# Kernel tuning notes

Measured on AMD Instinct MI355X. Metric: run time of the kernel, lower is better.

## Reference

```python
import jax, jax.numpy as jnp
import numpy as np

TOP_K = 4


def setup_inputs() -> dict:
    key = jax.random.key(0)
    k1, k2, k3 = jax.random.split(key, 3)
    T, H, E = 16384, 2880, 128
    hidden_states = jax.random.normal(k1, (T, H), dtype=jnp.float32)
    weight = jax.random.normal(k2, (E, H), dtype=jnp.float32) * 0.02
    bias = jax.random.normal(k3, (E,), dtype=jnp.float32) * 0.02
    return {"hidden_states": hidden_states, "weight": weight, "bias": bias}


def reference(hidden_states, weight, bias):
    # [T, H] @ [H, E] + [E] -> router logits [T, E]
    hidden_states = hidden_states.reshape(-1, weight.shape[1])
    router_logits = jnp.einsum('th,eh->te', hidden_states, weight) + bias
    # top-k over experts, then softmax over the k selected logits
    router_top_value, router_indices = jax.lax.top_k(router_logits, TOP_K)
    router_scores = jax.nn.softmax(router_top_value, axis=-1)
    return router_scores, router_indices
```

## Files before the change

kernel.cpp:

```cpp
#include <hip/hip_runtime.h>
#include <hip/hip_bf16.h>
#include <math.h>

#define T_TOKENS 16384
#define H_DIM    2880
#define KHALF    1440
#define E_EXP    128
#define TOPK     4
#define MT       32
#define MTM      64
#define KC       32
#define NCHUNK   (H_DIM / KC)
#define NCHUNK_H (KHALF / KC)
#define EPS_GAP  5e-4f

#define WS_WOFF   64
#define WS_WBYTES (NCHUNK * 1024 * 16)
#define WS_FLOFF  (WS_WOFF + WS_WBYTES)
#define WS_CAOFF  (WS_FLOFF + T_TOKENS * 4)
#define WS_NEED   (WS_CAOFF + T_TOKENS * 8)

typedef __bf16 bf16x8 __attribute__((ext_vector_type(8)));
typedef float  f32x4  __attribute__((ext_vector_type(4)));

__device__ __forceinline__ void split2(float a, float b,
                                       unsigned int& hi, unsigned int& lo) {
    float2 p; p.x = a; p.y = b;
    __hip_bfloat162 h = __float22bfloat162_rn(p);
    unsigned int hu; __builtin_memcpy(&hu, &h, 4);
    float2 r;
    r.x = a - __uint_as_float((hu & 0xffffu) << 16);
    r.y = b - __uint_as_float(hu & 0xffff0000u);
    __hip_bfloat162 l = __float22bfloat162_rn(r);
    unsigned int lu; __builtin_memcpy(&lu, &l, 4);
    hi = hu; lo = lu;
}

__global__ __launch_bounds__(256) void prep_w(const float* __restrict__ W,
                                              uint4* __restrict__ wsW) {
    const int f   = blockIdx.x * 256 + threadIdx.x;
    const int kc  = f >> 9;
    const int rem = f & 511;
    const int nt  = rem >> 6;
    const int L   = rem & 63;
    const int e   = nt * 16 + (L & 15);
    const int k   = kc * KC + (L >> 4) * 8;
    const float* p = W + (size_t)e * H_DIM + k;
    const float4 x0 = *(const float4*)p;
    const float4 x1 = *(const float4*)(p + 4);
    uint4 hi, lo;
    split2(x0.x, x0.y, hi.x, lo.x);
    split2(x0.z, x0.w, hi.y, lo.y);
    split2(x1.x, x1.y, hi.z, lo.z);
    split2(x1.z, x1.w, hi.w, lo.w);
    wsW[(size_t)kc * 1024 + nt * 64 + L]       = hi;
    wsW[(size_t)kc * 1024 + 512 + nt * 64 + L] = lo;
}

__global__ __launch_bounds__(1024, 4) void router_main(
    const float* __restrict__ A, const uint4* __restrict__ wsW,
    const float* __restrict__ bias, float* __restrict__ out,
    int* __restrict__ flag_count, int* __restrict__ flag_list,
    uint2* __restrict__ cand_list)
{
    union SMem {
        struct {
            uint4 W  [2][2][1024];
            uint4 Ahi[2][2][4][64];
            uint4 Alo[2][2][4][64];
        } s;
        float L[MTM][129];
    };
    __shared__ SMem sm;

    const int tid    = threadIdx.x;
    const int t_base = blockIdx.x * MTM;

    const int wave  = tid >> 6;
    const int L     = tid & 63;
    const int whalf = wave >> 3;
    const int wmg   = (wave >> 2) & 1;
    const int wng   = wave & 3;

    const int shalf = whalf;
    const int wv    = wave & 7;
    const uint4* wsrc = wsW + (size_t)(shalf * NCHUNK_H) * 1024 + (wv * 2) * 64 + L;

    const bool doA = tid < 512;
    const int ah   = wave & 1;
    const int awm  = (wave >> 1) & 3;
    const int akq  = L >> 4;
    const int t16  = L & 15;
    const int at   = awm * 16 + t16;
    const float* Ag = A + (size_t)(t_base + at) * H_DIM + ah * KHALF + akq * 8;

    f32x4 acc[2][2];
#pragma unroll
    for (int m = 0; m < 2; ++m)
#pragma unroll
        for (int n = 0; n < 2; ++n) { f32x4 z = {0.f, 0.f, 0.f, 0.f}; acc[m][n] = z; }

#define STAGE(NB, IT)                                                          \
    {                                                                          \
        if (doA) {                                                             \
            uint4 hi4, lo4;                                                    \
            split2(av0.x, av0.y, hi4.x, lo4.x);                                \
            split2(av0.z, av0.w, hi4.y, lo4.y);                                \
            split2(av1.x, av1.y, hi4.z, lo4.z);                                \
            split2(av1.z, av1.w, hi4.w, lo4.w);                                \
            sm.s.Ahi[NB][ah][awm][L] = hi4;                                    \
            sm.s.Alo[NB][ah][awm][L] = lo4;                                    \
        }                                                                      \
        const uint4* wc = wsrc + (size_t)(IT) * 1024;                          \
        _Pragma("unroll")                                                      \
        for (int j = 0; j < 2; ++j) {                                          \
            __builtin_amdgcn_global_load_lds(                                  \
                (const __attribute__((address_space(1))) void*)(wc + j * 64),  \
                (__attribute__((address_space(3))) void*)&sm.s.W[NB][shalf][(wv * 2 + j) * 64], \
                16, 0, 0);                                                     \
        }                                                                      \
    }

    float4 av0, av1;
    if (doA) { av0 = *(const float4*)(Ag); av1 = *(const float4*)(Ag + 4); }
    STAGE(0, 0);
    if (doA) { av0 = *(const float4*)(Ag + KC); av1 = *(const float4*)(Ag + KC + 4); }
    __syncthreads();

    int b = 0;
    for (int it = 0; it < NCHUNK_H; ++it) {
        if (it + 1 < NCHUNK_H) {
            STAGE(b ^ 1, it + 1);
            if (doA && it + 2 < NCHUNK_H) {
                av0 = *(const float4*)(Ag + (it + 2) * KC);
                av1 = *(const float4*)(Ag + (it + 2) * KC + 4);
            }
        }
        const bf16x8 ah0 = *(const bf16x8*)&sm.s.Ahi[b][whalf][wmg * 2 + 0][L];
        const bf16x8 al0 = *(const bf16x8*)&sm.s.Alo[b][whalf][wmg * 2 + 0][L];
        const bf16x8 ah1 = *(const bf16x8*)&sm.s.Ahi[b][whalf][wmg * 2 + 1][L];
        const bf16x8 al1 = *(const bf16x8*)&sm.s.Alo[b][whalf][wmg * 2 + 1][L];
#pragma unroll
        for (int n = 0; n < 2; ++n) {
            const int nt = wng * 2 + n;
            const bf16x8 whi = *(const bf16x8*)&sm.s.W[b][whalf][nt * 64 + L];
            const bf16x8 wlo = *(const bf16x8*)&sm.s.W[b][whalf][512 + nt * 64 + L];
            acc[0][n] = __builtin_amdgcn_mfma_f32_16x16x32_bf16(ah0, whi, acc[0][n], 0, 0, 0);
            acc[0][n] = __builtin_amdgcn_mfma_f32_16x16x32_bf16(ah0, wlo, acc[0][n], 0, 0, 0);
            acc[0][n] = __builtin_amdgcn_mfma_f32_16x16x32_bf16(al0, whi, acc[0][n], 0, 0, 0);
            acc[1][n] = __builtin_amdgcn_mfma_f32_16x16x32_bf16(ah1, whi, acc[1][n], 0, 0, 0);
            acc[1][n] = __builtin_amdgcn_mfma_f32_16x16x32_bf16(ah1, wlo, acc[1][n], 0, 0, 0);
            acc[1][n] = __builtin_amdgcn_mfma_f32_16x16x32_bf16(al1, whi, acc[1][n], 0, 0, 0);
        }
        __syncthreads();
        b ^= 1;
    }
#undef STAGE

    if (whalf == 0) {
#pragma unroll
        for (int m = 0; m < 2; ++m)
#pragma unroll
            for (int n = 0; n < 2; ++n) {
                const int e = (wng * 2 + n) * 16 + (L & 15);
                const float bv = bias[e];
#pragma unroll
                for (int r = 0; r < 4; ++r)
                    sm.L[(wmg * 2 + m) * 16 + (L >> 4) * 4 + r][e] = acc[m][n][r] + bv;
            }
    }
    __syncthreads();
    if (whalf == 1) {
#pragma unroll
        for (int m = 0; m < 2; ++m)
#pragma unroll
            for (int n = 0; n < 2; ++n) {
                const int e = (wng * 2 + n) * 16 + (L & 15);
#pragma unroll
                for (int r = 0; r < 4; ++r)
                    sm.L[(wmg * 2 + m) * 16 + (L >> 4) * 4 + r][e] += acc[m][n][r];
            }
    }
    __syncthreads();

    if (tid < MTM) {
        float v0 = -1e30f, v1 = -1e30f, v2 = -1e30f, v3 = -1e30f, v4 = -1e30f;
        int   i0 = 0, i1 = 0, i2 = 0, i3 = 0, i4 = 0;
        for (int e = 0; e < E_EXP; ++e) {
            const float x = sm.L[tid][e];
            if (x > v4) {
                if (x > v0)      { v4=v3;i4=i3; v3=v2;i3=i2; v2=v1;i2=i1; v1=v0;i1=i0; v0=x;i0=e; }
                else if (x > v1) { v4=v3;i4=i3; v3=v2;i3=i2; v2=v1;i2=i1; v1=x;i1=e; }
                else if (x > v2) { v4=v3;i4=i3; v3=v2;i3=i2; v2=x;i2=e; }
                else if (x > v3) { v4=v3;i4=i3; v3=x;i3=e; }
                else             { v4=x;i4=e; }
            }
        }
        const float g0 = v0 - v1, g1 = v1 - v2, g2 = v2 - v3, g3 = v3 - v4;
        float mg = g0 < g1 ? g0 : g1;
        mg = mg < g2 ? mg : g2;
        mg = mg < g3 ? mg : g3;

        const float e0x = expf(v0 - v0);
        const float e1x = expf(v1 - v0);
        const float e2x = expf(v2 - v0);
        const float e3x = expf(v3 - v0);
        const float s   = e0x + e1x + e2x + e3x;

        const int gt = t_base + tid;
        float* out_scores = out;
        float* out_idx    = out + (size_t)T_TOKENS * TOPK;
        out_scores[gt * 4 + 0] = e0x / s;
        out_scores[gt * 4 + 1] = e1x / s;
        out_scores[gt * 4 + 2] = e2x / s;
        out_scores[gt * 4 + 3] = e3x / s;
        out_idx[gt * 4 + 0] = (float)i0;
        out_idx[gt * 4 + 1] = (float)i1;
        out_idx[gt * 4 + 2] = (float)i2;
        out_idx[gt * 4 + 3] = (float)i3;

        if (mg < EPS_GAP) {
            const int p = atomicAdd(flag_count, 1);
            if (p < T_TOKENS) {
                flag_list[p] = gt;
                unsigned ids[8];
                int nc = 0;
                const float thr = v3 - EPS_GAP;
                for (int e = 0; e < E_EXP; ++e) {
                    if (sm.L[tid][e] >= thr) {
                        if (nc < 8) ids[nc] = (unsigned)e;
                        ++nc;
                    }
                }
                uint2 cd;
                if (nc > 8) {
                    cd.x = 0xFEu; cd.y = 0xFFFFFFFFu;
                } else {
                    for (int q = nc; q < 8; ++q) ids[q] = 0xFFu;
                    cd.x = ids[0] | (ids[1] << 8) | (ids[2] << 16) | (ids[3] << 24);
                    cd.y = ids[4] | (ids[5] << 8) | (ids[6] << 16) | (ids[7] << 24);
                }
                cand_list[p] = cd;
            }
        }
    }
}

__global__ __launch_bounds__(256) void router_recheck(
    const float* __restrict__ A, const float* __restrict__ W,
    const float* __restrict__ bias, float* __restrict__ out,
    const int* __restrict__ flag_count, const int* __restrict__ flag_list,
    const uint2* __restrict__ cand_list)
{
    __shared__ float  sA[H_DIM];
    __shared__ double sLog[8];
    __shared__ int    sIds[8];
    __shared__ double sPart[256];
    __shared__ double sFull[E_EXP];

    int count = *flag_count;
    if (count > T_TOKENS) count = T_TOKENS;

    const int tid = threadIdx.x;

    for (int i = blockIdx.x; i < count; i += gridDim.x) {
        const int t = flag_list[i];
        const uint2 cd = cand_list[i];
        __syncthreads();

        for (int q = tid; q < H_DIM / 4; q += 256)
            *(float4*)&sA[q * 4] = *(const float4*)(A + (size_t)t * H_DIM + q * 4);
        __syncthreads();

        const bool full = ((cd.x & 0xFFu) == 0xFEu);
        if (!full) {
            const int sl = tid >> 5;
            const int j  = tid & 31;
            const unsigned e = (sl < 4 ? (cd.x >> (sl * 8)) : (cd.y >> ((sl - 4) * 8))) & 0xFFu;
            double sum = 0.0;
            if (e < E_EXP) {
                const float* wrow = W + (size_t)e * H_DIM;
                for (int k = j; k < H_DIM; k += 32)
                    sum += (double)sA[k] * (double)wrow[k];
            }
#pragma unroll
            for (int off = 16; off > 0; off >>= 1)
                sum += __shfl_down(sum, off, 32);
            if (j == 0) {
                sIds[sl] = (e < E_EXP) ? (int)e : -1;
                sLog[sl] = (e < E_EXP) ? (sum + (double)bias[e]) : -1e300;
            }
            __syncthreads();
            if (tid == 0) {
                double v0 = -1e300, v1 = -1e300, v2 = -1e300, v3 = -1e300;
                int    i0 = 0, i1 = 0, i2 = 0, i3 = 0;
                for (int q = 0; q < 8; ++q) {
                    if (sIds[q] < 0) continue;
                    const double x = sLog[q];
                    const int    id = sIds[q];
                    if (x > v3) {
                        if (x > v0)      { v3=v2;i3=i2; v2=v1;i2=i1; v1=v0;i1=i0; v0=x;i0=id; }
                        else if (x > v1) { v3=v2;i3=i2; v2=v1;i2=i1; v1=x;i1=id; }
                        else if (x > v2) { v3=v2;i3=i2; v2=x;i2=id; }
                        else             { v3=x;i3=id; }
                    }
                }
                const double e0x = exp(v0 - v0);
                const double e1x = exp(v1 - v0);
                const double e2x = exp(v2 - v0);
                const double e3x = exp(v3 - v0);
                const double s   = e0x + e1x + e2x + e3x;
                float* out_scores = out;
                float* out_idx    = out + (size_t)T_TOKENS * TOPK;
                out_scores[t * 4 + 0] = (float)(e0x / s);
                out_scores[t * 4 + 1] = (float)(e1x / s);
                out_scores[t * 4 + 2] = (float)(e2x / s);
                out_scores[t * 4 + 3] = (float)(e3x / s);
                out_idx[t * 4 + 0] = (float)i0;
                out_idx[t * 4 + 1] = (float)i1;
                out_idx[t * 4 + 2] = (float)i2;
                out_idx[t * 4 + 3] = (float)i3;
            }
        } else {
            const int e = tid & (E_EXP - 1);
            const int h = tid >> 7;
            const float* wrow = W + (size_t)e * H_DIM + h * KHALF;
            const float* arow = &sA[h * KHALF];
            double s0 = 0.0, s1 = 0.0;
            for (int k = 0; k < KHALF; k += 2) {
                s0 += (double)arow[k]     * (double)wrow[k];
                s1 += (double)arow[k + 1] * (double)wrow[k + 1];
            }
            sPart[tid] = s0 + s1;
            __syncthreads();
            if (h == 0) sFull[e] = sPart[e] + sPart[e + 128] + (double)bias[e];
            __syncthreads();
            if (tid == 0) {
                double v0 = -1e300, v1 = -1e300, v2 = -1e300, v3 = -1e300;
                int    i0 = 0, i1 = 0, i2 = 0, i3 = 0;
                for (int q = 0; q < E_EXP; ++q) {
                    const double x = sFull[q];
                    if (x > v3) {
                        if (x > v0)      { v3=v2;i3=i2; v2=v1;i2=i1; v1=v0;i1=i0; v0=x;i0=q; }
                        else if (x > v1) { v3=v2;i3=i2; v2=v1;i2=i1; v1=x;i1=q; }
                        else if (x > v2) { v3=v2;i3=i2; v2=x;i2=q; }
                        else             { v3=x;i3=q; }
                    }
                }
                const double e0x = exp(v0 - v0);
                const double e1x = exp(v1 - v0);
                const double e2x = exp(v2 - v0);
                const double e3x = exp(v3 - v0);
                const double s   = e0x + e1x + e2x + e3x;
                float* out_scores = out;
                float* out_idx    = out + (size_t)T_TOKENS * TOPK;
                out_scores[t * 4 + 0] = (float)(e0x / s);
                out_scores[t * 4 + 1] = (float)(e1x / s);
                out_scores[t * 4 + 2] = (float)(e2x / s);
                out_scores[t * 4 + 3] = (float)(e3x / s);
                out_idx[t * 4 + 0] = (float)i0;
                out_idx[t * 4 + 1] = (float)i1;
                out_idx[t * 4 + 2] = (float)i2;
                out_idx[t * 4 + 3] = (float)i3;
            }
        }
        __syncthreads();
    }
}

__global__ __launch_bounds__(512, 4) void router_main_fb(
    const float* __restrict__ A, const float* __restrict__ W,
    const float* __restrict__ bias, float* __restrict__ out,
    int* __restrict__ flag_count, int* __restrict__ flag_list)
{
    __shared__ __align__(16) uint2 sAhi[2][2][128];
    __shared__ __align__(16) uint2 sAlo[2][2][128];
    __shared__ __align__(16) uint4 sWhi[2][8][64];
    __shared__ __align__(16) uint4 sWlo[2][8][64];
    __shared__ float sL[MT][129];

    const int tid    = threadIdx.x;
    const int t_base = blockIdx.x * MT;
    const int wave  = tid >> 6;
    const int L     = tid & 63;
    const int whalf = wave >> 2;
    const int wm    = wave & 1;
    const int wn    = (wave >> 1) & 1;
    const int shalf = tid >> 8;
    const int tid_h = tid & 255;
    const int at = tid_h >> 3;
    const int ac = tid_h & 7;
    const int a_idx = (at >> 4) * 128 + ((((ac >> 1) << 4) | (at & 15)) << 1) + (ac & 1);
    const float* Ag = A + (size_t)(t_base + at) * H_DIM + shalf * KHALF + ac * 4;
    const int we  = tid_h >> 1;
    const int wq0 = (tid_h & 1) * 2;
    const float* Wg = W + (size_t)we * H_DIM + shalf * KHALF + wq0 * 8;
    const int w_nt = we >> 4;
    const int w_n  = we & 15;

    uint2* sAhiF = &sAhi[shalf][0][0];
    uint2* sAloF = &sAlo[shalf][0][0];

    f32x4 acc[4];
#pragma unroll
    for (int i = 0; i < 4; ++i) { f32x4 z = {0.f, 0.f, 0.f, 0.f}; acc[i] = z; }

    for (int k0 = 0; k0 < KHALF; k0 += KC) {
        const float4 av  = *(const float4*)(Ag + k0);
        const float4 wv0 = *(const float4*)(Wg + k0);
        const float4 wv1 = *(const float4*)(Wg + k0 + 4);
        const float4 wv2 = *(const float4*)(Wg + k0 + 8);
        const float4 wv3 = *(const float4*)(Wg + k0 + 12);

        uint2 ahp, alp;
        split2(av.x, av.y, ahp.x, alp.x);
        split2(av.z, av.w, ahp.y, alp.y);
        uint4 whp0, wlp0, whp1, wlp1;
        split2(wv0.x, wv0.y, whp0.x, wlp0.x);
        split2(wv0.z, wv0.w, whp0.y, wlp0.y);
        split2(wv1.x, wv1.y, whp0.z, wlp0.z);
        split2(wv1.z, wv1.w, whp0.w, wlp0.w);
        split2(wv2.x, wv2.y, whp1.x, wlp1.x);
        split2(wv2.z, wv2.w, whp1.y, wlp1.y);
        split2(wv3.x, wv3.y, whp1.z, wlp1.z);
        split2(wv3.z, wv3.w, whp1.w, wlp1.w);

        __syncthreads();
        sAhiF[a_idx] = ahp;
        sAloF[a_idx] = alp;
        sWhi[shalf][w_nt][((wq0 + 0) << 4) | w_n] = whp0;
        sWhi[shalf][w_nt][((wq0 + 1) << 4) | w_n] = whp1;
        sWlo[shalf][w_nt][((wq0 + 0) << 4) | w_n] = wlp0;
        sWlo[shalf][w_nt][((wq0 + 1) << 4) | w_n] = wlp1;
        __syncthreads();

        const bf16x8 ahi = *(const bf16x8*)&sAhi[whalf][wm][L * 2];
        const bf16x8 alo = *(const bf16x8*)&sAlo[whalf][wm][L * 2];
#pragma unroll
        for (int i = 0; i < 4; ++i) {
            const int nt = wn * 4 + i;
            const bf16x8 whi = *(const bf16x8*)&sWhi[whalf][nt][L];
            const bf16x8 wlo = *(const bf16x8*)&sWlo[whalf][nt][L];
            acc[i] = __builtin_amdgcn_mfma_f32_16x16x32_bf16(ahi, whi, acc[i], 0, 0, 0);
            acc[i] = __builtin_amdgcn_mfma_f32_16x16x32_bf16(ahi, wlo, acc[i], 0, 0, 0);
            acc[i] = __builtin_amdgcn_mfma_f32_16x16x32_bf16(alo, whi, acc[i], 0, 0, 0);
        }
    }

    __syncthreads();
    if (whalf == 0) {
#pragma unroll
        for (int i = 0; i < 4; ++i) {
            const int e = wn * 64 + i * 16 + (L & 15);
            const float b = bias[e];
#pragma unroll
            for (int r = 0; r < 4; ++r)
                sL[wm * 16 + (L >> 4) * 4 + r][e] = acc[i][r] + b;
        }
    }
    __syncthreads();
    if (whalf == 1) {
#pragma unroll
        for (int i = 0; i < 4; ++i) {
            const int e = wn * 64 + i * 16 + (L & 15);
#pragma unroll
            for (int r = 0; r < 4; ++r)
                sL[wm * 16 + (L >> 4) * 4 + r][e] += acc[i][r];
        }
    }
    __syncthreads();

    if (tid < MT) {
        float v0 = -1e30f, v1 = -1e30f, v2 = -1e30f, v3 = -1e30f, v4 = -1e30f;
        int   i0 = 0, i1 = 0, i2 = 0, i3 = 0, i4 = 0;
        for (int e = 0; e < E_EXP; ++e) {
            const float x = sL[tid][e];
            if (x > v4) {
                if (x > v0)      { v4=v3;i4=i3; v3=v2;i3=i2; v2=v1;i2=i1; v1=v0;i1=i0; v0=x;i0=e; }
                else if (x > v1) { v4=v3;i4=i3; v3=v2;i3=i2; v2=v1;i2=i1; v1=x;i1=e; }
                else if (x > v2) { v4=v3;i4=i3; v3=v2;i3=i2; v2=x;i2=e; }
                else if (x > v3) { v4=v3;i4=i3; v3=x;i3=e; }
                else             { v4=x;i4=e; }
            }
        }
        const float g0 = v0 - v1, g1 = v1 - v2, g2 = v2 - v3, g3 = v3 - v4;
        float mg = g0 < g1 ? g0 : g1;
        mg = mg < g2 ? mg : g2;
        mg = mg < g3 ? mg : g3;

        const float e0x = expf(v0 - v0);
        const float e1x = expf(v1 - v0);
        const float e2x = expf(v2 - v0);
        const float e3x = expf(v3 - v0);
        const float s   = e0x + e1x + e2x + e3x;

        const int gt = t_base + tid;
        float* out_scores = out;
        float* out_idx    = out + (size_t)T_TOKENS * TOPK;
        out_scores[gt * 4 + 0] = e0x / s;
        out_scores[gt * 4 + 1] = e1x / s;
        out_scores[gt * 4 + 2] = e2x / s;
        out_scores[gt * 4 + 3] = e3x / s;
        out_idx[gt * 4 + 0] = (float)i0;
        out_idx[gt * 4 + 1] = (float)i1;
        out_idx[gt * 4 + 2] = (float)i2;
        out_idx[gt * 4 + 3] = (float)i3;

        if (mg < EPS_GAP) {
            const int p = atomicAdd(flag_count, 1);
            if (p < T_TOKENS) flag_list[p] = gt;
        }
    }
}

__global__ __launch_bounds__(256) void router_recheck_fb(
    const float* __restrict__ A, const float* __restrict__ W,
    const float* __restrict__ bias, float* __restrict__ out,
    const int* __restrict__ flag_count, const int* __restrict__ flag_list)
{
    __shared__ double sPart[256];
    __shared__ double sLog[E_EXP];

    int count = *flag_count;
    if (count > T_TOKENS) count = T_TOKENS;

    const int tid = threadIdx.x;
    const int e   = tid & (E_EXP - 1);
    const int h   = tid >> 7;

    for (int i = blockIdx.x; i < count; i += gridDim.x) {
        const int t = flag_list[i];
        const float* arow = A + (size_t)t * H_DIM + h * KHALF;
        const float* wrow = W + (size_t)e * H_DIM + h * KHALF;

        double s0 = 0.0, s1 = 0.0, s2 = 0.0, s3 = 0.0;
        float4 a[8], w[8];
#pragma unroll
        for (int q = 0; q < 8; ++q) {
            a[q] = *(const float4*)(arow + q * 4);
            w[q] = *(const float4*)(wrow + q * 4);
        }
        for (int it = 0; it < KHALF / 32 - 1; ++it) {
            const float* ap = arow + (it + 1) * 32;
            const float* wp = wrow + (it + 1) * 32;
            float4 na[8], nw[8];
#pragma unroll
            for (int q = 0; q < 8; ++q) {
                na[q] = *(const float4*)(ap + q * 4);
                nw[q] = *(const float4*)(wp + q * 4);
            }
#pragma unroll
            for (int q = 0; q < 8; ++q) {
                s0 += (double)a[q].x * (double)w[q].x;
                s1 += (double)a[q].y * (double)w[q].y;
                s2 += (double)a[q].z * (double)w[q].z;
                s3 += (double)a[q].w * (double)w[q].w;
            }
#pragma unroll
            for (int q = 0; q < 8; ++q) { a[q] = na[q]; w[q] = nw[q]; }
        }
#pragma unroll
        for (int q = 0; q < 8; ++q) {
            s0 += (double)a[q].x * (double)w[q].x;
            s1 += (double)a[q].y * (double)w[q].y;
            s2 += (double)a[q].z * (double)w[q].z;
            s3 += (double)a[q].w * (double)w[q].w;
        }
        sPart[tid] = (s0 + s1) + (s2 + s3);
        __syncthreads();
        if (h == 0) sLog[e] = sPart[e] + sPart[e + 128] + (double)bias[e];
        __syncthreads();

        if (tid == 0) {
            double v0 = -1e300, v1 = -1e300, v2 = -1e300, v3 = -1e300;
            int    i0 = 0, i1 = 0, i2 = 0, i3 = 0;
            for (int q = 0; q < E_EXP; ++q) {
                const double x = sLog[q];
                if (x > v3) {
                    if (x > v0)      { v3=v2;i3=i2; v2=v1;i2=i1; v1=v0;i1=i0; v0=x;i0=q; }
                    else if (x > v1) { v3=v2;i3=i2; v2=v1;i2=i1; v1=x;i1=q; }
                    else if (x > v2) { v3=v2;i3=i2; v2=x;i2=q; }
                    else             { v3=x;i3=q; }
                }
            }
            const double e0x = exp(v0 - v0);
            const double e1x = exp(v1 - v0);
            const double e2x = exp(v2 - v0);
            const double e3x = exp(v3 - v0);
            const double s   = e0x + e1x + e2x + e3x;
            float* out_scores = out;
            float* out_idx    = out + (size_t)T_TOKENS * TOPK;
            out_scores[t * 4 + 0] = (float)(e0x / s);
            out_scores[t * 4 + 1] = (float)(e1x / s);
            out_scores[t * 4 + 2] = (float)(e2x / s);
            out_scores[t * 4 + 3] = (float)(e3x / s);
            out_idx[t * 4 + 0] = (float)i0;
            out_idx[t * 4 + 1] = (float)i1;
            out_idx[t * 4 + 2] = (float)i2;
            out_idx[t * 4 + 3] = (float)i3;
        }
        __syncthreads();
    }
}

extern "C" void kernel_launch(void* const* d_in, const int* in_sizes, int n_in,
                              void* d_out, int out_size, void* d_ws, size_t ws_size,
                              hipStream_t stream) {
    const float* A    = (const float*)d_in[0];
    const float* W    = (const float*)d_in[1];
    const float* bias = (const float*)d_in[2];
    float* out = (float*)d_out;

    if (ws_size >= (size_t)WS_NEED) {
        int*   flag_count = (int*)d_ws;
        uint4* wsW        = (uint4*)((char*)d_ws + WS_WOFF);
        int*   flag_list  = (int*)((char*)d_ws + WS_FLOFF);
        uint2* cand_list  = (uint2*)((char*)d_ws + WS_CAOFF);
        hipMemsetAsync(flag_count, 0, sizeof(int), stream);
        prep_w<<<dim3((NCHUNK * 512) / 256), dim3(256), 0, stream>>>(W, wsW);
        router_main<<<dim3(T_TOKENS / MTM), dim3(1024), 0, stream>>>(
            A, wsW, bias, out, flag_count, flag_list, cand_list);
        router_recheck<<<dim3(512), dim3(256), 0, stream>>>(
            A, W, bias, out, flag_count, flag_list, cand_list);
    } else {
        int* flag_count = (int*)d_ws;
        int* flag_list  = (int*)d_ws + 1;
        hipMemsetAsync(flag_count, 0, sizeof(int), stream);
        router_main_fb<<<dim3(T_TOKENS / MT), dim3(512), 0, stream>>>(A, W, bias, out,
                                                                      flag_count, flag_list);
        router_recheck_fb<<<dim3(512), dim3(256), 0, stream>>>(A, W, bias, out,
                                                               flag_count, flag_list);
    }
}
```

Measured before the change: 354.9 us.

## Spread A loads across all threads and use fine-grained vmcnt barriers

The A-tile staging now uses all 1024 threads, each loading one float4 instead of 512 threads loading two. The main loop is restructured with explicit s_waitcnt vmcnt(1) plus s_barrier and sched_barrier fences, and the last iterations are peeled. A global prefetch for the next chunk can therefore stay in flight across the barrier while the current chunk's MFMAs run. The risk is that the hand-placed waitcnt counts are fragile if the compiler reorders or emits extra memory operations.

New measurement: 344.2 us. -3.0%, faster.

```diff
diff --git a/kernel.cpp b/kernel.cpp
--- a/kernel.cpp
+++ b/kernel.cpp
@@ -86,13 +86,14 @@
     const int wv    = wave & 7;
     const uint4* wsrc = wsW + (size_t)(shalf * NCHUNK_H) * 1024 + (wv * 2) * 64 + L;
 
-    const bool doA = tid < 512;
-    const int ah   = wave & 1;
-    const int awm  = (wave >> 1) & 3;
-    const int akq  = L >> 4;
-    const int t16  = L & 15;
-    const int at   = awm * 16 + t16;
-    const float* Ag = A + (size_t)(t_base + at) * H_DIM + ah * KHALF + akq * 8;
+    const int at   = tid >> 4;
+    const int kq   = tid & 15;
+    const int ah   = kq >> 3;
+    const int oct  = (kq >> 1) & 3;
+    const int sub  = kq & 1;
+    const int amt  = at >> 4;
+    const int t16  = at & 15;
+    const float* Ag = A + (size_t)(t_base + at) * H_DIM + ah * KHALF + oct * 8 + sub * 4;
 
     f32x4 acc[2][2];
 #pragma unroll
@@ -100,62 +101,85 @@
 #pragma unroll
         for (int n = 0; n < 2; ++n) { f32x4 z = {0.f, 0.f, 0.f, 0.f}; acc[m][n] = z; }
 
-#define STAGE(NB, IT)                                                          \
+#define GLDS(SRC, DST) \
+    __builtin_amdgcn_global_load_lds( \
+        (const __attribute__((address_space(1))) void*)(SRC), \
+        (__attribute__((address_space(3))) void*)(DST), 16, 0, 0)
+
+#define STAGE_W(NB, IT)                                                        \
     {                                                                          \
-        if (doA) {                                                             \
-            uint4 hi4, lo4;                                                    \
-            split2(av0.x, av0.y, hi4.x, lo4.x);                                \
-            split2(av0.z, av0.w, hi4.y, lo4.y);                                \
-            split2(av1.x, av1.y, hi4.z, lo4.z);                                \
-            split2(av1.z, av1.w, hi4.w, lo4.w);                                \
-            sm.s.Ahi[NB][ah][awm][L] = hi4;                                    \
-            sm.s.Alo[NB][ah][awm][L] = lo4;                                    \
+        const uint4* wc = wsrc + (size_t)(IT) * 1024;                          \
+        GLDS(wc,      &sm.s.W[NB][shalf][(wv * 2 + 0) * 64]);                  \
+        GLDS(wc + 64, &sm.s.W[NB][shalf][(wv * 2 + 1) * 64]);                  \
+    }
+
+#define STAGE_A(NB)                                                            \
+    {                                                                          \
+        uint2 h2, l2;                                                          \
+        split2(av.x, av.y, h2.x, l2.x);                                        \
+        split2(av.z, av.w, h2.y, l2.y);                                        \
+        ((uint2*)&sm.s.Ahi[NB][ah][amt][oct * 16 + t16])[sub] = h2;            \
+        ((uint2*)&sm.s.Alo[NB][ah][amt][oct * 16 + t16])[sub] = l2;            \
+    }
+
+#define COMPUTE(NB)                                                            \
+    {                                                                          \
+        const bf16x8 ah0 = *(const bf16x8*)&sm.s.Ahi[NB][whalf][wmg * 2 + 0][L]; \
+        const bf16x8 al0 = *(const bf16x8*)&sm.s.Alo[NB][whalf][wmg * 2 + 0][L]; \
+        const bf16x8 ah1 = *(const bf16x8*)&sm.s.Ahi[NB][whalf][wmg * 2 + 1][L]; \
+        const bf16x8 al1 = *(const bf16x8*)&sm.s.Alo[NB][whalf][wmg * 2 + 1][L]; \
+        _Pragma("unroll")                                                      \
+        for (int n = 0; n < 2; ++n) {                                          \
+            const int nt = wng * 2 + n;                                        \
+            const bf16x8 whi = *(const bf16x8*)&sm.s.W[NB][whalf][nt * 64 + L]; \
+            const bf16x8 wlo = *(const bf16x8*)&sm.s.W[NB][whalf][512 + nt * 64 + L]; \
+            acc[0][n] = __builtin_amdgcn_mfma_f32_16x16x32_bf16(ah0, whi, acc[0][n], 0, 0, 0); \
+            acc[0][n] = __builtin_amdgcn_mfma_f32_16x16x32_bf16(ah0, wlo, acc[0][n], 0, 0, 0); \
+            acc[0][n] = __builtin_amdgcn_mfma_f32_16x16x32_bf16(al0, whi, acc[0][n], 0, 0, 0); \
+            acc[1][n] = __builtin_amdgcn_mfma_f32_16x16x32_bf16(ah1, whi, acc[1][n], 0, 0, 0); \
+            acc[1][n] = __builtin_amdgcn_mfma_f32_16x16x32_bf16(ah1, wlo, acc[1][n], 0, 0, 0); \
+            acc[1][n] = __builtin_amdgcn_mfma_f32_16x16x32_bf16(al1, whi, acc[1][n], 0, 0, 0); \
         }                                                                      \
-        const uint4* wc = wsrc + (size_t)(IT) * 1024;                          \
-        _Pragma("unroll")                                                      \
-        for (int j = 0; j < 2; ++j) {                                          \
-            __builtin_amdgcn_global_load_lds(                                  \
-                (const __attribute__((address_space(1))) void*)(wc + j * 64),  \
-                (__attribute__((address_space(3))) void*)&sm.s.W[NB][shalf][(wv * 2 + j) * 64], \
-                16, 0, 0);                                                     \
-        }                                                                      \
-    }
-
-    float4 av0, av1;
-    if (doA) { av0 = *(const float4*)(Ag); av1 = *(const float4*)(Ag + 4); }
-    STAGE(0, 0);
-    if (doA) { av0 = *(const float4*)(Ag + KC); av1 = *(const float4*)(Ag + KC + 4); }
+    }
+
+#define CBAR(VM)                                                               \
+    asm volatile("s_waitcnt vmcnt(" #VM ") lgkmcnt(0)" ::: "memory");          \
+    __builtin_amdgcn_s_barrier();                                              \
+    __builtin_amdgcn_sched_barrier(0);
+
+    float4 av = *(const float4*)Ag;
+    STAGE_A(0);
+    STAGE_W(0, 0);
+    __builtin_amdgcn_sched_barrier(0);
+    av = *(const float4*)(Ag + KC);
+    CBAR(1)
+
+    int b = 0;
+    for (int it = 0; it < NCHUNK_H - 2; ++it) {
+        STAGE_W(b ^ 1, it + 1);
+        __builtin_amdgcn_sched_barrier(0);
+        const float4 avn = *(const float4*)(Ag + (it + 2) * KC);
+        STAGE_A(b ^ 1);
+        av = avn;
+        COMPUTE(b);
+        CBAR(1)
+        b ^= 1;
+    }
+    {
+        STAGE_W(b ^ 1, NCHUNK_H - 1);
+        STAGE_A(b ^ 1);
+        COMPUTE(b);
+        CBAR(0)
+        b ^= 1;
+    }
+    COMPUTE(b);
     __syncthreads();
 
-    int b = 0;
-    for (int it = 0; it < NCHUNK_H; ++it) {
-        if (it + 1 < NCHUNK_H) {
-            STAGE(b ^ 1, it + 1);
-            if (doA && it + 2 < NCHUNK_H) {
-                av0 = *(const float4*)(Ag + (it + 2) * KC);
-                av1 = *(const float4*)(Ag + (it + 2) * KC + 4);
-            }
-        }
-        const bf16x8 ah0 = *(const bf16x8*)&sm.s.Ahi[b][whalf][wmg * 2 + 0][L];
-        const bf16x8 al0 = *(const bf16x8*)&sm.s.Alo[b][whalf][wmg * 2 + 0][L];
-        const bf16x8 ah1 = *(const bf16x8*)&sm.s.Ahi[b][whalf][wmg * 2 + 1][L];
-        const bf16x8 al1 = *(const bf16x8*)&sm.s.Alo[b][whalf][wmg * 2 + 1][L];
-#pragma unroll
-        for (int n = 0; n < 2; ++n) {
-            const int nt = wng * 2 + n;
-            const bf16x8 whi = *(const bf16x8*)&sm.s.W[b][whalf][nt * 64 + L];
-            const bf16x8 wlo = *(const bf16x8*)&sm.s.W[b][whalf][512 + nt * 64 + L];
-            acc[0][n] = __builtin_amdgcn_mfma_f32_16x16x32_bf16(ah0, whi, acc[0][n], 0, 0, 0);
-            acc[0][n] = __builtin_amdgcn_mfma_f32_16x16x32_bf16(ah0, wlo, acc[0][n], 0, 0, 0);
-            acc[0][n] = __builtin_amdgcn_mfma_f32_16x16x32_bf16(al0, whi, acc[0][n], 0, 0, 0);
-            acc[1][n] = __builtin_amdgcn_mfma_f32_16x16x32_bf16(ah1, whi, acc[1][n], 0, 0, 0);
-            acc[1][n] = __builtin_amdgcn_mfma_f32_16x16x32_bf16(ah1, wlo, acc[1][n], 0, 0, 0);
-            acc[1][n] = __builtin_amdgcn_mfma_f32_16x16x32_bf16(al1, whi, acc[1][n], 0, 0, 0);
-        }
-        __syncthreads();
-        b ^= 1;
-    }
-#undef STAGE
+#undef GLDS
+#undef STAGE_W
+#undef STAGE_A
+#undef COMPUTE
+#undef CBAR
 
     if (whalf == 0) {
 #pragma unroll
```
